# Optimization experiments

Measured on AMD Instinct MI355X. Metric: run time of the kernel, lower is better.

## Reference

```python
import jax, jax.numpy as jnp
import numpy as np

NBINS = 256  # skimage threshold_otsu default
RGB_W = np.array([0.2989, 0.5870, 0.1140], dtype=np.float32)  # tf.image.rgb_to_grayscale weights


def setup_inputs() -> dict:
    key = jax.random.key(0)
    inputs = jax.random.uniform(key, (16, 1024, 1024, 3), dtype=jnp.float32)
    return {"inputs": inputs}


def _otsu_threshold(x_flat):
    # Histogram over [min, max] with NBINS bins (skimage semantics: one
    # global threshold over the whole array passed to threshold_otsu).
    mn = x_flat.min()
    mx = x_flat.max()
    width = (mx - mn) / NBINS
    idx = jnp.clip(((x_flat - mn) / width).astype(jnp.int32), 0, NBINS - 1)
    counts = jnp.zeros((NBINS,), jnp.float32).at[idx].add(1.0)
    centers = mn + width * (jnp.arange(NBINS, dtype=jnp.float32) + 0.5)

    # class-separation (between-class variance) per candidate split
    w1 = jnp.cumsum(counts)                      # weight of class 1 (<= t)
    w2 = jnp.cumsum(counts[::-1])[::-1]          # weight of class 2 (> t)
    s1 = jnp.cumsum(counts * centers)
    s2 = jnp.cumsum((counts * centers)[::-1])[::-1]
    m1 = s1 / jnp.maximum(w1, 1.0)
    m2 = s2 / jnp.maximum(w2, 1.0)
    var12 = w1[:-1] * w2[1:] * (m1[:-1] - m2[1:]) ** 2
    return centers[jnp.argmax(var12)]


def reference(inputs):
    # rgb -> grayscale (tf.image.rgb_to_grayscale weights), keep channel dim
    gray = jnp.einsum('bhwc,c->bhw', inputs[..., :3], jnp.asarray(RGB_W))[..., None]
    thresh = _otsu_threshold(gray.ravel())  # single global threshold over the whole batch
    return jnp.where(gray > thresh, 1.0, 0.0).astype(jnp.float32)
```

## Files before the change

### kernel.cpp

```cpp
#include <hip/hip_runtime.h>


static constexpr float W0 = 0.2989f;
static constexpr float W1 = 0.5870f;
static constexpr float W2 = 0.1140f;

static constexpr int GRAY_BLOCKS = 4096;
static constexpr int HIST_BLOCKS = 512;
static constexpr int BIN_BLOCKS  = 4096;

__device__ __forceinline__ float gray_of(float r, float g, float b) {
    return __fadd_rn(__fadd_rn(__fmul_rn(r, W0), __fmul_rn(g, W1)), __fmul_rn(b, W2));
}

__device__ __forceinline__ void wave_minmax(float& lmin, float& lmax) {
    #pragma unroll
    for (int off = 32; off > 0; off >>= 1) {
        lmin = fminf(lmin, __shfl_down(lmin, off));
        lmax = fmaxf(lmax, __shfl_down(lmax, off));
    }
}

__device__ __forceinline__ void reduce_partials(
        const float* __restrict__ pmin, const float* __restrict__ pmax,
        int n, int nthreads, float& out_mn, float& out_mx) {
    __shared__ float smin[16], smax[16];
    int t = threadIdx.x;
    float lmin = __uint_as_float(0x7f800000u);
    float lmax = -lmin;
    for (int i = t; i < n; i += nthreads) {
        lmin = fminf(lmin, pmin[i]);
        lmax = fmaxf(lmax, pmax[i]);
    }
    wave_minmax(lmin, lmax);
    int nw = nthreads >> 6;
    if ((t & 63) == 0) { smin[t >> 6] = lmin; smax[t >> 6] = lmax; }
    __syncthreads();
    float m = smin[0], M = smax[0];
    for (int w = 1; w < nw; ++w) { m = fminf(m, smin[w]); M = fmaxf(M, smax[w]); }
    out_mn = m; out_mx = M;
    __syncthreads();
}

__global__ __launch_bounds__(256) void k_gray(
        const float4* __restrict__ in4, float4* __restrict__ gray4,
        float* __restrict__ pmin, float* __restrict__ pmax,
        unsigned* __restrict__ done_ctr) {
    if (blockIdx.x == 0 && threadIdx.x == 0) *done_ctr = 0u;
    int t = threadIdx.x;
    int base = blockIdx.x * 1024;
    float lmin = __uint_as_float(0x7f800000u);
    float lmax = -lmin;
    #pragma unroll
    for (int j = 0; j < 4; ++j) {
        int g = base + j * 256 + t;
        const float4* src = in4 + 3 * (size_t)g;
        float4 a = src[0];
        float4 b = src[1];
        float4 c = src[2];
        float g0 = gray_of(a.x, a.y, a.z);
        float g1 = gray_of(a.w, b.x, b.y);
        float g2 = gray_of(b.z, b.w, c.x);
        float g3 = gray_of(c.y, c.z, c.w);
        float4 o; o.x = g0; o.y = g1; o.z = g2; o.w = g3;
        gray4[g] = o;
        lmin = fminf(lmin, fminf(fminf(g0, g1), fminf(g2, g3)));
        lmax = fmaxf(lmax, fmaxf(fmaxf(g0, g1), fmaxf(g2, g3)));
    }
    wave_minmax(lmin, lmax);
    __shared__ float smin[4], smax[4];
    if ((t & 63) == 0) { smin[t >> 6] = lmin; smax[t >> 6] = lmax; }
    __syncthreads();
    if (t == 0) {
        pmin[blockIdx.x] = fminf(fminf(smin[0], smin[1]), fminf(smin[2], smin[3]));
        pmax[blockIdx.x] = fmaxf(fmaxf(smax[0], smax[1]), fmaxf(smax[2], smax[3]));
    }
}

__global__ __launch_bounds__(256) void k_hist_otsu(
        const float4* __restrict__ gray4,
        const float* __restrict__ pmin, const float* __restrict__ pmax,
        unsigned* __restrict__ hist_part, unsigned* __restrict__ done_ctr,
        float* __restrict__ thresh, int npix4) {
    float mn, mx;
    reduce_partials(pmin, pmax, GRAY_BLOCKS, 256, mn, mx);
    float width = __fdiv_rn(__fsub_rn(mx, mn), 256.0f);

    __shared__ unsigned lh[1024];
    for (int j = threadIdx.x; j < 1024; j += 256) lh[j] = 0u;
    __syncthreads();
    unsigned* myh = &lh[(threadIdx.x >> 6) << 8];
    int stride = gridDim.x * 256;
    for (int i = blockIdx.x * 256 + threadIdx.x; i < npix4; i += stride) {
        float4 g = gray4[i];
        int i0 = (int)__fdiv_rn(__fsub_rn(g.x, mn), width);
        int i1 = (int)__fdiv_rn(__fsub_rn(g.y, mn), width);
        int i2 = (int)__fdiv_rn(__fsub_rn(g.z, mn), width);
        int i3 = (int)__fdiv_rn(__fsub_rn(g.w, mn), width);
        i0 = min(max(i0, 0), 255);
        i1 = min(max(i1, 0), 255);
        i2 = min(max(i2, 0), 255);
        i3 = min(max(i3, 0), 255);
        atomicAdd(&myh[i0], 1u);
        atomicAdd(&myh[i1], 1u);
        atomicAdd(&myh[i2], 1u);
        atomicAdd(&myh[i3], 1u);
    }
    __syncthreads();
    int b = threadIdx.x;
    hist_part[(size_t)blockIdx.x * 256 + b] =
        lh[b] + lh[256 + b] + lh[512 + b] + lh[768 + b];

    __threadfence();
    __shared__ unsigned lastflag;
    if (b == 0) {
        unsigned prev = __hip_atomic_fetch_add(
            done_ctr, 1u, __ATOMIC_ACQ_REL, __HIP_MEMORY_SCOPE_AGENT);
        lastflag = (prev == (unsigned)(gridDim.x - 1)) ? 1u : 0u;
    }
    __syncthreads();
    if (!lastflag) return;
    __threadfence();

    __shared__ float counts[256], centers[256], tt[256];
    __shared__ float w1[256], s1[256], w2[256], s2[256], vv[256];
    unsigned acc = 0;
    #pragma unroll 8
    for (int k = 0; k < HIST_BLOCKS; ++k)
        acc += hist_part[(size_t)k * 256 + b];
    counts[b] = (float)acc;
    centers[b] = __fadd_rn(mn, __fmul_rn(width, __fadd_rn((float)b, 0.5f)));
    tt[b] = __fmul_rn(counts[b], centers[b]);
    __syncthreads();
    if (b == 0) {
        float aw = 0.0f, as = 0.0f;
        #pragma unroll 16
        for (int i = 0; i < 256; ++i) {
            aw = __fadd_rn(aw, counts[i]); w1[i] = aw;
            as = __fadd_rn(as, tt[i]);     s1[i] = as;
        }
        aw = 0.0f; as = 0.0f;
        #pragma unroll 16
        for (int i = 255; i >= 0; --i) {
            aw = __fadd_rn(aw, counts[i]); w2[i] = aw;
            as = __fadd_rn(as, tt[i]);     s2[i] = as;
        }
    }
    __syncthreads();
    if (b < 255) {
        float m1 = __fdiv_rn(s1[b],     fmaxf(w1[b],     1.0f));
        float m2 = __fdiv_rn(s2[b + 1], fmaxf(w2[b + 1], 1.0f));
        float d  = __fsub_rn(m1, m2);
        vv[b] = __fmul_rn(__fmul_rn(w1[b], w2[b + 1]), __fmul_rn(d, d));
    }
    __syncthreads();
    if (b == 0) {
        float best = -1.0f; int bi = 0;
        #pragma unroll 16
        for (int i = 0; i < 255; ++i) {
            float v = vv[i];
            if (v > best) { best = v; bi = i; }
        }
        *thresh = centers[bi];
    }
}

__global__ __launch_bounds__(256) void k_bin(
        float4* __restrict__ g4, const float* __restrict__ thresh) {
    const float th = thresh[0];
    int t = threadIdx.x;
    int base = blockIdx.x * 1024;
    #pragma unroll
    for (int j = 0; j < 4; ++j) {
        int i = base + j * 256 + t;
        float4 g = g4[i];
        float4 o;
        o.x = g.x > th ? 1.0f : 0.0f;
        o.y = g.y > th ? 1.0f : 0.0f;
        o.z = g.z > th ? 1.0f : 0.0f;
        o.w = g.w > th ? 1.0f : 0.0f;
        g4[i] = o;
    }
}

extern "C" void kernel_launch(void* const* d_in, const int* in_sizes, int n_in,
                              void* d_out, int out_size, void* d_ws, size_t ws_size,
                              hipStream_t stream) {
    const float4* in4 = (const float4*)d_in[0];
    float4* gray4 = (float4*)d_out;

    int npix = in_sizes[0] / 3;
    int npix4 = npix / 4;

    float* pmin = (float*)d_ws;
    float* pmax = pmin + GRAY_BLOCKS;
    float* thresh = pmax + GRAY_BLOCKS;
    unsigned* done_ctr = (unsigned*)(thresh + 1);
    unsigned* hist_part = done_ctr + 1;

    k_gray<<<GRAY_BLOCKS, 256, 0, stream>>>(in4, gray4, pmin, pmax, done_ctr);
    k_hist_otsu<<<HIST_BLOCKS, 256, 0, stream>>>((const float4*)d_out, pmin, pmax,
                                                 hist_part, done_ctr, thresh, npix4);
    k_bin<<<BIN_BLOCKS, 256, 0, stream>>>(gray4, thresh);
}
```

Before: 405.2 us.

## Split Otsu threshold computation into separate single-block kernel

```diff
diff --git a/kernel.cpp b/kernel.cpp
--- a/kernel.cpp
+++ b/kernel.cpp
@@ -44,9 +44,7 @@
 
 __global__ __launch_bounds__(256) void k_gray(
         const float4* __restrict__ in4, float4* __restrict__ gray4,
-        float* __restrict__ pmin, float* __restrict__ pmax,
-        unsigned* __restrict__ done_ctr) {
-    if (blockIdx.x == 0 && threadIdx.x == 0) *done_ctr = 0u;
+        float* __restrict__ pmin, float* __restrict__ pmax) {
     int t = threadIdx.x;
     int base = blockIdx.x * 1024;
     float lmin = __uint_as_float(0x7f800000u);
@@ -77,11 +75,10 @@
     }
 }
 
-__global__ __launch_bounds__(256) void k_hist_otsu(
+__global__ __launch_bounds__(256) void k_hist(
         const float4* __restrict__ gray4,
         const float* __restrict__ pmin, const float* __restrict__ pmax,
-        unsigned* __restrict__ hist_part, unsigned* __restrict__ done_ctr,
-        float* __restrict__ thresh, int npix4) {
+        unsigned* __restrict__ hist_part, int npix4) {
     float mn, mx;
     reduce_partials(pmin, pmax, GRAY_BLOCKS, 256, mn, mx);
     float width = __fdiv_rn(__fsub_rn(mx, mn), 256.0f);
@@ -110,29 +107,35 @@
     int b = threadIdx.x;
     hist_part[(size_t)blockIdx.x * 256 + b] =
         lh[b] + lh[256 + b] + lh[512 + b] + lh[768 + b];
-
-    __threadfence();
-    __shared__ unsigned lastflag;
-    if (b == 0) {
-        unsigned prev = __hip_atomic_fetch_add(
-            done_ctr, 1u, __ATOMIC_ACQ_REL, __HIP_MEMORY_SCOPE_AGENT);
-        lastflag = (prev == (unsigned)(gridDim.x - 1)) ? 1u : 0u;
-    }
-    __syncthreads();
-    if (!lastflag) return;
-    __threadfence();
-
+}
+
+__global__ __launch_bounds__(1024) void k_otsu(
+        const unsigned* __restrict__ hist_part,
+        const float* __restrict__ pmin, const float* __restrict__ pmax,
+        float* __restrict__ thresh) {
+    float mn, mx;
+    reduce_partials(pmin, pmax, GRAY_BLOCKS, 1024, mn, mx);
+    float width = __fdiv_rn(__fsub_rn(mx, mn), 256.0f);
+
+    __shared__ unsigned csum[1024];
     __shared__ float counts[256], centers[256], tt[256];
     __shared__ float w1[256], s1[256], w2[256], s2[256], vv[256];
+    int t = threadIdx.x;
+    int b = t & 255, q = t >> 8;
     unsigned acc = 0;
     #pragma unroll 8
-    for (int k = 0; k < HIST_BLOCKS; ++k)
+    for (int k = q; k < HIST_BLOCKS; k += 4)
         acc += hist_part[(size_t)k * 256 + b];
-    counts[b] = (float)acc;
-    centers[b] = __fadd_rn(mn, __fmul_rn(width, __fadd_rn((float)b, 0.5f)));
-    tt[b] = __fmul_rn(counts[b], centers[b]);
-    __syncthreads();
-    if (b == 0) {
+    csum[q * 256 + b] = acc;
+    __syncthreads();
+    if (t < 256) {
+        unsigned c = csum[t] + csum[256 + t] + csum[512 + t] + csum[768 + t];
+        counts[t] = (float)c;
+        centers[t] = __fadd_rn(mn, __fmul_rn(width, __fadd_rn((float)t, 0.5f)));
+        tt[t] = __fmul_rn(counts[t], centers[t]);
+    }
+    __syncthreads();
+    if (t == 0) {
         float aw = 0.0f, as = 0.0f;
         #pragma unroll 16
         for (int i = 0; i < 256; ++i) {
@@ -147,14 +150,14 @@
         }
     }
     __syncthreads();
-    if (b < 255) {
-        float m1 = __fdiv_rn(s1[b],     fmaxf(w1[b],     1.0f));
-        float m2 = __fdiv_rn(s2[b + 1], fmaxf(w2[b + 1], 1.0f));
+    if (t < 255) {
+        float m1 = __fdiv_rn(s1[t],     fmaxf(w1[t],     1.0f));
+        float m2 = __fdiv_rn(s2[t + 1], fmaxf(w2[t + 1], 1.0f));
         float d  = __fsub_rn(m1, m2);
-        vv[b] = __fmul_rn(__fmul_rn(w1[b], w2[b + 1]), __fmul_rn(d, d));
-    }
-    __syncthreads();
-    if (b == 0) {
+        vv[t] = __fmul_rn(__fmul_rn(w1[t], w2[t + 1]), __fmul_rn(d, d));
+    }
+    __syncthreads();
+    if (t == 0) {
         float best = -1.0f; int bi = 0;
         #pragma unroll 16
         for (int i = 0; i < 255; ++i) {
@@ -195,11 +198,11 @@
     float* pmin = (float*)d_ws;
     float* pmax = pmin + GRAY_BLOCKS;
     float* thresh = pmax + GRAY_BLOCKS;
-    unsigned* done_ctr = (unsigned*)(thresh + 1);
-    unsigned* hist_part = done_ctr + 1;
-
-    k_gray<<<GRAY_BLOCKS, 256, 0, stream>>>(in4, gray4, pmin, pmax, done_ctr);
-    k_hist_otsu<<<HIST_BLOCKS, 256, 0, stream>>>((const float4*)d_out, pmin, pmax,
-                                                 hist_part, done_ctr, thresh, npix4);
+    unsigned* hist_part = (unsigned*)(thresh + 1);
+
+    k_gray<<<GRAY_BLOCKS, 256, 0, stream>>>(in4, gray4, pmin, pmax);
+    k_hist<<<HIST_BLOCKS, 256, 0, stream>>>((const float4*)d_out, pmin, pmax,
+                                            hist_part, npix4);
+    k_otsu<<<1, 1024, 0, stream>>>(hist_part, pmin, pmax, thresh);
     k_bin<<<BIN_BLOCKS, 256, 0, stream>>>(gray4, thresh);
 }
```

Result: faster. 356.8 us (median of 2 runs) (-11.9%).

## Replace last-block Otsu tail with redundant per-block threshold in binarize kernel

Applied to the files above, without the earlier changes.

```diff
diff --git a/kernel.cpp b/kernel.cpp
--- a/kernel.cpp
+++ b/kernel.cpp
@@ -7,7 +7,7 @@
 
 static constexpr int GRAY_BLOCKS = 4096;
 static constexpr int HIST_BLOCKS = 512;
-static constexpr int BIN_BLOCKS  = 4096;
+static constexpr int BIN_BLOCKS  = 512;
 
 __device__ __forceinline__ float gray_of(float r, float g, float b) {
     return __fadd_rn(__fadd_rn(__fmul_rn(r, W0), __fmul_rn(g, W1)), __fmul_rn(b, W2));
@@ -44,9 +44,7 @@
 
 __global__ __launch_bounds__(256) void k_gray(
         const float4* __restrict__ in4, float4* __restrict__ gray4,
-        float* __restrict__ pmin, float* __restrict__ pmax,
-        unsigned* __restrict__ done_ctr) {
-    if (blockIdx.x == 0 && threadIdx.x == 0) *done_ctr = 0u;
+        float* __restrict__ pmin, float* __restrict__ pmax) {
     int t = threadIdx.x;
     int base = blockIdx.x * 1024;
     float lmin = __uint_as_float(0x7f800000u);
@@ -77,11 +75,10 @@
     }
 }
 
-__global__ __launch_bounds__(256) void k_hist_otsu(
+__global__ __launch_bounds__(256) void k_hist(
         const float4* __restrict__ gray4,
         const float* __restrict__ pmin, const float* __restrict__ pmax,
-        unsigned* __restrict__ hist_part, unsigned* __restrict__ done_ctr,
-        float* __restrict__ thresh, int npix4) {
+        unsigned* __restrict__ hist_part, int npix4) {
     float mn, mx;
     reduce_partials(pmin, pmax, GRAY_BLOCKS, 256, mn, mx);
     float width = __fdiv_rn(__fsub_rn(mx, mn), 256.0f);
@@ -110,20 +107,19 @@
     int b = threadIdx.x;
     hist_part[(size_t)blockIdx.x * 256 + b] =
         lh[b] + lh[256 + b] + lh[512 + b] + lh[768 + b];
+}
 
-    __threadfence();
-    __shared__ unsigned lastflag;
-    if (b == 0) {
-        unsigned prev = __hip_atomic_fetch_add(
-            done_ctr, 1u, __ATOMIC_ACQ_REL, __HIP_MEMORY_SCOPE_AGENT);
-        lastflag = (prev == (unsigned)(gridDim.x - 1)) ? 1u : 0u;
-    }
-    __syncthreads();
-    if (!lastflag) return;
-    __threadfence();
+__global__ __launch_bounds__(256) void k_bin_otsu(
+        float4* __restrict__ g4, const unsigned* __restrict__ hist_part,
+        const float* __restrict__ pmin, const float* __restrict__ pmax) {
+    float mn, mx;
+    reduce_partials(pmin, pmax, GRAY_BLOCKS, 256, mn, mx);
+    float width = __fdiv_rn(__fsub_rn(mx, mn), 256.0f);
 
     __shared__ float counts[256], centers[256], tt[256];
     __shared__ float w1[256], s1[256], w2[256], s2[256], vv[256];
+    __shared__ float sth;
+    int b = threadIdx.x;
     unsigned acc = 0;
     #pragma unroll 8
     for (int k = 0; k < HIST_BLOCKS; ++k)
@@ -161,18 +157,15 @@
             float v = vv[i];
             if (v > best) { best = v; bi = i; }
         }
-        *thresh = centers[bi];
+        sth = centers[bi];
     }
-}
+    __syncthreads();
+    const float th = sth;
 
-__global__ __launch_bounds__(256) void k_bin(
-        float4* __restrict__ g4, const float* __restrict__ thresh) {
-    const float th = thresh[0];
-    int t = threadIdx.x;
-    int base = blockIdx.x * 1024;
-    #pragma unroll
-    for (int j = 0; j < 4; ++j) {
-        int i = base + j * 256 + t;
+    int base = blockIdx.x * 8192;
+    #pragma unroll 4
+    for (int j = 0; j < 32; ++j) {
+        int i = base + j * 256 + b;
         float4 g = g4[i];
         float4 o;
         o.x = g.x > th ? 1.0f : 0.0f;
@@ -194,12 +187,10 @@
 
     float* pmin = (float*)d_ws;
     float* pmax = pmin + GRAY_BLOCKS;
-    float* thresh = pmax + GRAY_BLOCKS;
-    unsigned* done_ctr = (unsigned*)(thresh + 1);
-    unsigned* hist_part = done_ctr + 1;
+    unsigned* hist_part = (unsigned*)(pmax + GRAY_BLOCKS);
 
-    k_gray<<<GRAY_BLOCKS, 256, 0, stream>>>(in4, gray4, pmin, pmax, done_ctr);
-    k_hist_otsu<<<HIST_BLOCKS, 256, 0, stream>>>((const float4*)d_out, pmin, pmax,
-                                                 hist_part, done_ctr, thresh, npix4);
-    k_bin<<<BIN_BLOCKS, 256, 0, stream>>>(gray4, thresh);
+    k_gray<<<GRAY_BLOCKS, 256, 0, stream>>>(in4, gray4, pmin, pmax);
+    k_hist<<<HIST_BLOCKS, 256, 0, stream>>>((const float4*)d_out, pmin, pmax,
+                                            hist_part, npix4);
+    k_bin_otsu<<<BIN_BLOCKS, 256, 0, stream>>>(gray4, hist_part, pmin, pmax);
 }
```

New measurement: 363.7 us. -10.2%, faster.
